# Optimization experiments

Measured on AMD Instinct MI355X. Metric: run time of the kernel, lower is better.

## Reference

```python
import jax, jax.numpy as jnp
import numpy as np

NUM_EXPERTS = 8
TOP_K = 2
LORA_ALPHA = 2.0
LORA_RANK = 16
D_MODEL = 2048
D_HIDDEN = 5632


def setup_inputs() -> dict:
    key = jax.random.key(0)
    ks = jax.random.split(key, 11)
    B, S, D, H, E, R = 2, 1024, D_MODEL, D_HIDDEN, NUM_EXPERTS, LORA_RANK
    sd = 1.0 / np.sqrt(D)
    sh = 1.0 / np.sqrt(H)
    x = jax.random.normal(ks[0], (B, S, D), jnp.float32)
    gate_w = jax.random.normal(ks[1], (E, D), jnp.float32) * sd   # router Linear(D->E), no bias
    w_up = jax.random.normal(ks[2], (H, D), jnp.float32) * sd     # up_proj.weight
    w_gate = jax.random.normal(ks[3], (H, D), jnp.float32) * sd   # gate_proj.weight
    w_down = jax.random.normal(ks[4], (D, H), jnp.float32) * sh   # down_proj.weight
    up_A = jax.random.normal(ks[5], (E, R, D), jnp.float32) * sd
    up_B = jax.random.normal(ks[6], (E, H, R), jnp.float32) * 0.02
    gate_A = jax.random.normal(ks[7], (E, R, D), jnp.float32) * sd
    gate_B = jax.random.normal(ks[8], (E, H, R), jnp.float32) * 0.02
    down_A = jax.random.normal(ks[9], (E, R, H), jnp.float32) * sh
    down_B = jax.random.normal(ks[10], (E, D, R), jnp.float32) * 0.02
    return {"x": x, "gate_w": gate_w, "w_up": w_up, "w_gate": w_gate,
            "w_down": w_down, "up_A": up_A, "up_B": up_B,
            "gate_A": gate_A, "gate_B": gate_B, "down_A": down_A, "down_B": down_B}


def reference(x, gate_w, w_up, w_gate, w_down, up_A, up_B, gate_A, gate_B, down_A, down_B):
    B, S, D = x.shape
    H = w_up.shape[0]
    # router: logits [B,S,E], top-k over experts (last dim)
    gate_logits = jnp.einsum('bsd,ed->bse', x, gate_w)
    topw, sel = jax.lax.top_k(gate_logits, TOP_K)            # [B,S,k]
    # NOTE: source applies softmax over dim=1 (the SEQUENCE axis) -- reproduced faithfully
    topw = jax.nn.softmax(topw.astype(jnp.float32), axis=1).astype(x.dtype)
    xt = x.reshape(-1, D)                                    # [T, D]
    wf = topw.reshape(-1, TOP_K)                             # [T, k]
    sf = sel.reshape(-1, TOP_K)                              # [T, k]
    # shared base projections computed once for all tokens
    base_up = xt @ w_up.T                                    # [T, H]
    base_gate = xt @ w_gate.T                                # [T, H]
    mixed_h = jnp.zeros((xt.shape[0], H), x.dtype)
    lora_down = jnp.zeros_like(xt)
    # loop over fixed small expert count; low-rank LoRA deltas applied without
    # materializing full merged weights (same math by linearity of matmul)
    for e in range(NUM_EXPERTS):
        c = jnp.sum(jnp.where(sf == e, wf, 0.0), axis=1)     # [T] routing weight (0 if not routed)
        lo_up = LORA_ALPHA * ((xt @ up_A[e].T) @ up_B[e].T)
        lo_gate = LORA_ALPHA * ((xt @ gate_A[e].T) @ gate_B[e].T)
        h_e = jax.nn.silu(base_up + lo_up) * (base_gate + lo_gate)  # [T, H]
        ch = c[:, None] * h_e
        mixed_h = mixed_h + ch
        lora_down = lora_down + LORA_ALPHA * ((ch @ down_A[e].T) @ down_B[e].T)
    out = mixed_h @ w_down.T + lora_down                     # base down GEMM done once on mixed hidden
    return out.reshape(B, S, D)
```

## Files before the change

kernel.cpp:

```cpp
#include <hip/hip_runtime.h>
#include <hip/hip_fp16.h>
#include <cmath>

#define TOKENS 2048
#define DMODEL 2048
#define DHID   5632
#define NEXP   8
#define RANK   16
#define LALPHA 2.0f

typedef __attribute__((ext_vector_type(4))) float f32x4;
typedef __attribute__((ext_vector_type(8))) short s16x8;
typedef __attribute__((ext_vector_type(4))) short s16x4;
typedef __attribute__((ext_vector_type(8))) _Float16 f16x8;

__device__ __forceinline__ short f2bf(float f){
  unsigned u = __float_as_uint(f);
  u += 0x7fffu + ((u >> 16) & 1u);
  return (short)(u >> 16);
}
__device__ __forceinline__ short f2h(float f){
  return (short)__half_as_ushort(__float2half(f));
}

struct Src2 { const short* s0; const short* s1; };

__device__ __forceinline__ Src2 mk_src(const short* g, long ld, int tid){
  Src2 st;
  const int L0 = tid,      r0 = L0>>2, c0 = ((L0&3) - (r0>>1)) & 3;
  const int L1 = 256+tid,  r1 = L1>>2, c1 = ((L1&3) - (r1>>1)) & 3;
  st.s0 = g + (long)r0*ld + c0*8;
  st.s1 = g + (long)r1*ld + c1*8;
  return st;
}
__device__ __forceinline__ void stage2(const Src2& st, int k0, short* t, int tid){
  __builtin_amdgcn_global_load_lds((const __attribute__((address_space(1))) void*)(st.s0 + k0),
                                   (__attribute__((address_space(3))) void*)(t + tid*8), 16, 0, 0);
  __builtin_amdgcn_global_load_lds((const __attribute__((address_space(1))) void*)(st.s1 + k0),
                                   (__attribute__((address_space(3))) void*)(t + (256+tid)*8), 16, 0, 0);
}
__device__ __forceinline__ s16x8 fragb(const short* t, int row, int quad){
  const int p = (quad + (row>>1)) & 3;
  return *(const s16x8*)(t + (row*4 + p)*8);
}
__device__ __forceinline__ f16x8 fragh(const short* t, int row, int quad){
  const int p = (quad + (row>>1)) & 3;
  return *(const f16x8*)(t + (row*4 + p)*8);
}

struct Stage64 { const short* g; short* t; int off[4]; int dof; };

__device__ __forceinline__ Stage64 mk_stage64(const short* g, long ld, short* t, int tid){
  Stage64 st; st.g = g; st.t = t;
  #pragma unroll
  for(int p=0;p<4;p++){
    const int L = p*256 + tid;
    const int r = L>>3, cp = L&7;
    const int c = (cp - (r&7)) & 7;
    st.off[p] = r*(int)ld + c*8;
  }
  st.dof = tid*8;
  return st;
}
__device__ __forceinline__ void do_stage64(const Stage64& st, int k0){
  #pragma unroll
  for(int p=0;p<4;p++)
    __builtin_amdgcn_global_load_lds(
      (const __attribute__((address_space(1))) void*)(st.g + st.off[p] + k0),
      (__attribute__((address_space(3))) void*)(st.t + st.dof + p*2048), 16, 0, 0);
}
__device__ __forceinline__ s16x8 fragb64(const short* t, int row, int ksub, int quad){
  const int c = ksub*4 + quad;
  const int p = (c + (row&7)) & 7;
  return *(const s16x8*)(t + (row*8 + p)*8);
}
__device__ __forceinline__ f16x8 fragh64(const short* t, int row, int ksub, int quad){
  const int c = ksub*4 + quad;
  const int p = (c + (row&7)) & 7;
  return *(const f16x8*)(t + (row*8 + p)*8);
}

__global__ void k_cast(const float* __restrict__ x, const float* __restrict__ w_up,
                       const float* __restrict__ w_gate, const float* __restrict__ w_down,
                       const float* __restrict__ upA, const float* __restrict__ gateA,
                       const float* __restrict__ downA, const float* __restrict__ upB,
                       const float* __restrict__ gateB, const float* __restrict__ downB,
                       short* __restrict__ xb, short* __restrict__ wub, short* __restrict__ wgb,
                       short* __restrict__ wdb, short* __restrict__ daA, short* __restrict__ acat,
                       short* __restrict__ upBcat, short* __restrict__ gateBcat, short* __restrict__ wdbcat){
  const long e0 = 4194304, e1 = 15728640, e2 = 27262976, e3 = 38797312;
  const long e4 = 39518208, e5 = 40042496, e6 = 40763392, e7 = 41484288, e8 = 41746432;
  const long i = ((long)blockIdx.x*256 + threadIdx.x) * 4;
  if(i >= e8) return;
  const float* src; short* dst; long l; int fp16 = 0;
  if(i < e0){ src = x; dst = xb; l = i; }
  else if(i < e1){ src = w_up; dst = wub; l = i - e0; }
  else if(i < e2){ src = w_gate; dst = wgb; l = i - e1; }
  else if(i < e3){ src = w_down; dst = wdb; l = i - e2; }
  else if(i < e4){ src = downA; dst = daA; l = i - e3; }
  else if(i < e5){
    l = i - e4;
    const long c = l>>11;
    const long e = c>>5, pj = (c>>4)&1, r = c&15;
    src = (pj ? gateA : upA) + ((e*RANK + r)<<11) + (l&2047) - l;
    dst = acat;
  }
  else if(i < e6){
    l = i - e5;
    const long h = l>>7, c = l&127, e = c>>4, r = c&15;
    src = upB + ((e*DHID + h)*RANK + r) - l;
    dst = upBcat; fp16 = 1;
  }
  else if(i < e7){
    l = i - e6;
    const long h = l>>7, c = l&127, e = c>>4, r = c&15;
    src = gateB + ((e*DHID + h)*RANK + r) - l;
    dst = gateBcat; fp16 = 1;
  }
  else {
    l = i - e7;
    const long d = l>>7, c = l&127, e = c>>4, r = c&15;
    src = downB + ((e*DMODEL + d)*RANK + r) - l;
    dst = wdbcat; fp16 = 1;
  }
  const float4 v = *(const float4*)(src + l);
  s16x4 o;
  if(fp16){ o[0]=f2h(v.x); o[1]=f2h(v.y); o[2]=f2h(v.z); o[3]=f2h(v.w); }
  else    { o[0]=f2bf(v.x); o[1]=f2bf(v.y); o[2]=f2bf(v.z); o[3]=f2bf(v.w); }
  *(s16x4*)(dst + l) = o;
}

__global__ void k_router(const float* __restrict__ x, const float* __restrict__ gw,
                         int* __restrict__ sel, float* __restrict__ topv){
  const int t = blockIdx.x*4 + (threadIdx.x>>6);
  const int lane = threadIdx.x & 63;
  const float* xr = x + (long)t * DMODEL;
  float acc[NEXP];
  #pragma unroll
  for(int e=0;e<NEXP;e++) acc[e]=0.f;
  #pragma unroll
  for(int it=0; it<8; it++){
    const int d = it*256 + lane*4;
    const float4 xv = *(const float4*)(xr + d);
    #pragma unroll
    for(int e=0;e<NEXP;e++){
      const float4 wv = *(const float4*)(gw + e*DMODEL + d);
      acc[e] += xv.x*wv.x + xv.y*wv.y + xv.z*wv.z + xv.w*wv.w;
    }
  }
  #pragma unroll
  for(int e=0;e<NEXP;e++){
    #pragma unroll
    for(int off=32; off; off>>=1) acc[e] += __shfl_down(acc[e], off, 64);
  }
  if(lane==0){
    int i0=0;
    #pragma unroll
    for(int e=1;e<NEXP;e++) if(acc[e]>acc[i0]) i0=e;
    int i1=-1;
    #pragma unroll
    for(int e=0;e<NEXP;e++){ if(e==i0) continue; if(i1<0 || acc[e]>acc[i1]) i1=e; }
    sel[t*2+0]=i0; sel[t*2+1]=i1;
    topv[t*2+0]=acc[i0]; topv[t*2+1]=acc[i1];
  }
}

__global__ void k_softmax(const float* __restrict__ topv, float* __restrict__ cw){
  const int b = blockIdx.x >> 1, k = blockIdx.x & 1;
  const int base = b*1024;
  __shared__ float red[256];
  float v[4];
  float mx = -1e30f;
  #pragma unroll
  for(int i=0;i<4;i++){
    int s = threadIdx.x + i*256;
    v[i] = topv[(base+s)*2 + k];
    mx = fmaxf(mx, v[i]);
  }
  red[threadIdx.x]=mx; __syncthreads();
  for(int o=128;o;o>>=1){ if(threadIdx.x<o) red[threadIdx.x]=fmaxf(red[threadIdx.x],red[threadIdx.x+o]); __syncthreads(); }
  mx = red[0]; __syncthreads();
  float sum=0.f;
  #pragma unroll
  for(int i=0;i<4;i++){ v[i]=__expf(v[i]-mx); sum+=v[i]; }
  red[threadIdx.x]=sum; __syncthreads();
  for(int o=128;o;o>>=1){ if(threadIdx.x<o) red[threadIdx.x]+=red[threadIdx.x+o]; __syncthreads(); }
  const float inv = 1.f/red[0];
  #pragma unroll
  for(int i=0;i<4;i++){
    int s = threadIdx.x + i*256;
    cw[(base+s)*2+k] = v[i]*inv;
  }
}

__global__ __launch_bounds__(256,2) void k_rank(
    const short* __restrict__ xb, const short* __restrict__ acat, float* __restrict__ Rall){
  __shared__ __align__(16) short At[8192];
  __shared__ __align__(16) short Bt[8192];
  const int c0 = blockIdx.x*128, t0 = blockIdx.y*128;
  const int kbeg = blockIdx.z*256;
  const int tid = threadIdx.x, lane = tid&63, wave = tid>>6;
  const int wm=(wave>>1)*64, wn=(wave&1)*64, fr=lane&15, quad=lane>>4;
  f32x4 acc[4][4];
  #pragma unroll
  for(int i=0;i<4;i++)
    #pragma unroll
    for(int j=0;j<4;j++) acc[i][j]=(f32x4){0.f,0.f,0.f,0.f};
  const Stage64 sA = mk_stage64(xb + (long)t0*DMODEL, DMODEL, At, tid);
  const Stage64 sB = mk_stage64(acat + (long)c0*DMODEL, DMODEL, Bt, tid);
  for(int k0=kbeg; k0<kbeg+256; k0+=64){
    do_stage64(sA, k0); do_stage64(sB, k0);
    __syncthreads();
    #pragma unroll
    for(int s=0;s<2;s++){
      s16x8 af[4];
      #pragma unroll
      for(int i=0;i<4;i++) af[i] = fragb64(At, wm + i*16 + fr, s, quad);
      #pragma unroll
      for(int j=0;j<4;j++){
        const s16x8 bf = fragb64(Bt, wn + j*16 + fr, s, quad);
        #pragma unroll
        for(int i=0;i<4;i++)
          acc[i][j] = __builtin_amdgcn_mfma_f32_16x16x32_bf16(af[i], bf, acc[i][j], 0,0,0);
      }
    }
    __syncthreads();
  }
  #pragma unroll
  for(int i=0;i<4;i++)
    #pragma unroll
    for(int j=0;j<4;j++){
      const int rbase = wm + i*16 + quad*4, col = wn + j*16 + fr;
      #pragma unroll
      for(int reg=0;reg<4;reg++)
        atomicAdd(&Rall[(long)(t0+rbase+reg)*256 + c0 + col], acc[i][j][reg]);
    }
}

__global__ void k_rsel(const float* __restrict__ Rall, const int* __restrict__ sel,
                       short* __restrict__ RselU, short* __restrict__ RselG){
  const int idx = blockIdx.x*256 + threadIdx.x;
  const int c = idx & 127, t = (idx>>7) & (TOKENS-1), k = idx>>18;
  const int e = c>>4, r = c&15;
  const int s = sel[t*2+k];
  const int m = (e==s);
  RselU[idx] = f2h(m ? LALPHA*Rall[(long)t*256 + e*32 + r]      : 0.f);
  RselG[idx] = f2h(m ? LALPHA*Rall[(long)t*256 + e*32 + 16 + r] : 0.f);
}

__global__ __launch_bounds__(256,2) void k_lora(
    const short* __restrict__ RselU, const short* __restrict__ RselG,
    const short* __restrict__ upBcat, const short* __restrict__ gateBcat,
    short* __restrict__ LF){
  __shared__ __align__(16) short At[8192];
  __shared__ __align__(16) short Gt[8192];
  __shared__ __align__(16) short Bt[8192];
  const int h0 = blockIdx.x*128, t0 = blockIdx.y*128;
  const short* Rsel = blockIdx.z ? RselG : RselU;
  const short* Bcat = blockIdx.z ? gateBcat : upBcat;
  const int tid = threadIdx.x, lane = tid&63, wave = tid>>6;
  const int wm=(wave>>1)*64, wn=(wave&1)*64, fr=lane&15, quad=lane>>4;
  f32x4 l0[4][4], l1[4][4];
  #pragma unroll
  for(int i=0;i<4;i++)
    #pragma unroll
    for(int j=0;j<4;j++){ l0[i][j]=(f32x4){0.f,0.f,0.f,0.f}; l1[i][j]=l0[i][j]; }
  const Stage64 sB  = mk_stage64(Bcat + (long)h0*128, 128, Bt, tid);
  const Stage64 sR0 = mk_stage64(Rsel + (long)t0*128, 128, At, tid);
  const Stage64 sR1 = mk_stage64(Rsel + ((long)TOKENS + t0)*128, 128, Gt, tid);
  for(int k0=0; k0<128; k0+=64){
    do_stage64(sB, k0); do_stage64(sR0, k0); do_stage64(sR1, k0);
    __syncthreads();
    #pragma unroll
    for(int s=0;s<2;s++){
      f16x8 a0[4], a1[4];
      #pragma unroll
      for(int i=0;i<4;i++){ a0[i] = fragh64(At, wm + i*16 + fr, s, quad);
                            a1[i] = fragh64(Gt, wm + i*16 + fr, s, quad); }
      #pragma unroll
      for(int j=0;j<4;j++){
        const f16x8 bf = fragh64(Bt, wn + j*16 + fr, s, quad);
        #pragma unroll
        for(int i=0;i<4;i++){
          l0[i][j] = __builtin_amdgcn_mfma_f32_16x16x32_f16(a0[i], bf, l0[i][j], 0,0,0);
          l1[i][j] = __builtin_amdgcn_mfma_f32_16x16x32_f16(a1[i], bf, l1[i][j], 0,0,0);
        }
      }
    }
    __syncthreads();
  }
  short* o = LF + (long)(blockIdx.y*44 + blockIdx.x)*65536 + ((long)blockIdx.z*16*256 + tid)*8;
  #pragma unroll
  for(int i=0;i<4;i++){
    s16x8 p0a, p0b, p1a, p1b;
    #pragma unroll
    for(int r=0;r<4;r++){
      p0a[r]   = f2h(l0[i][0][r]); p0a[4+r] = f2h(l0[i][1][r]);
      p0b[r]   = f2h(l0[i][2][r]); p0b[4+r] = f2h(l0[i][3][r]);
      p1a[r]   = f2h(l1[i][0][r]); p1a[4+r] = f2h(l1[i][1][r]);
      p1b[r]   = f2h(l1[i][2][r]); p1b[4+r] = f2h(l1[i][3][r]);
    }
    *(s16x8*)(o + (i*2+0)*2048)     = p0a;
    *(s16x8*)(o + (i*2+1)*2048)     = p0b;
    *(s16x8*)(o + (8 + i*2+0)*2048) = p1a;
    *(s16x8*)(o + (8 + i*2+1)*2048) = p1b;
  }
}

__global__ __launch_bounds__(256,2) void k_main(
    const short* __restrict__ xb, const short* __restrict__ wub, const short* __restrict__ wgb,
    const short* __restrict__ LF,
    const float* __restrict__ cw, unsigned short* __restrict__ ch, unsigned short* __restrict__ chsum){
  __shared__ __align__(16) short At[2][4096];
  __shared__ __align__(16) short Ut[2][4096];
  __shared__ __align__(16) short Gt[2][4096];
  __shared__ float cwv[128][2];
  const int h0 = blockIdx.x*128, t0 = blockIdx.y*128;
  const int tid = threadIdx.x, lane = tid&63, wave = tid>>6;
  const int wm=(wave>>1)*64, wn=(wave&1)*64, fr=lane&15, quad=lane>>4;
  { const int tl = tid>>1, k = tid&1; cwv[tl][k] = cw[(t0+tl)*2 + k]; }
  f32x4 au[4][4], ag[4][4];
  #pragma unroll
  for(int i=0;i<4;i++)
    #pragma unroll
    for(int j=0;j<4;j++){ au[i][j]=(f32x4){0.f,0.f,0.f,0.f}; ag[i][j]=au[i][j]; }
  const Src2 sA = mk_src(xb + (long)t0*DMODEL, DMODEL, tid);
  const Src2 sU = mk_src(wub + (long)h0*DMODEL, DMODEL, tid);
  const Src2 sG = mk_src(wgb + (long)h0*DMODEL, DMODEL, tid);
  stage2(sA, 0, At[0], tid); stage2(sU, 0, Ut[0], tid); stage2(sG, 0, Gt[0], tid);
  __syncthreads();
  int cur = 0;
  for(int k0=0; k0<DMODEL; k0+=32){
    const int nxt = cur^1;
    if(k0+32 < DMODEL){
      stage2(sA, k0+32, At[nxt], tid);
      stage2(sU, k0+32, Ut[nxt], tid);
      stage2(sG, k0+32, Gt[nxt], tid);
    }
    __builtin_amdgcn_sched_barrier(0);
    s16x8 af[4];
    #pragma unroll
    for(int i=0;i<4;i++) af[i] = fragb(At[cur], wm + i*16 + fr, quad);
    #pragma unroll
    for(int j=0;j<4;j++){
      const s16x8 bu = fragb(Ut[cur], wn + j*16 + fr, quad);
      const s16x8 bg = fragb(Gt[cur], wn + j*16 + fr, quad);
      #pragma unroll
      for(int i=0;i<4;i++){
        au[i][j] = __builtin_amdgcn_mfma_f32_16x16x32_bf16(af[i], bu, au[i][j], 0,0,0);
        ag[i][j] = __builtin_amdgcn_mfma_f32_16x16x32_bf16(af[i], bg, ag[i][j], 0,0,0);
      }
    }
    __syncthreads();
    cur = nxt;
  }
  const short* Lf = LF + (long)(blockIdx.y*44 + blockIdx.x)*65536 + (long)tid*8;
  #pragma unroll
  for(int i=0;i<4;i++){
    f16x8 Uv0[2], Uv1[2], Gv0[2], Gv1[2];
    Uv0[0] = *(const f16x8*)(Lf + (i*2+0)*2048);       Uv0[1] = *(const f16x8*)(Lf + (i*2+1)*2048);
    Uv1[0] = *(const f16x8*)(Lf + (8+i*2+0)*2048);     Uv1[1] = *(const f16x8*)(Lf + (8+i*2+1)*2048);
    Gv0[0] = *(const f16x8*)(Lf + (16+i*2+0)*2048);    Gv0[1] = *(const f16x8*)(Lf + (16+i*2+1)*2048);
    Gv1[0] = *(const f16x8*)(Lf + (24+i*2+0)*2048);    Gv1[1] = *(const f16x8*)(Lf + (24+i*2+1)*2048);
    #pragma unroll
    for(int reg=0;reg<4;reg++){
      const int tl = wm + i*16 + quad*4 + reg;
      const float c0 = cwv[tl][0], c1 = cwv[tl][1];
      const long row0 = (long)(t0+tl)*DHID + h0;
      const long row1 = ((long)TOKENS + t0+tl)*DHID + h0;
      unsigned short* r0 = ch + row0;
      unsigned short* r1 = ch + row1;
      unsigned short* rs = chsum + row0;
      #pragma unroll
      for(int j=0;j<4;j++){
        const int hl = wn + j*16 + fr;
        const int q = (j&1)*4 + reg, hv = j>>1;
        const float u0 = au[i][j][reg] + (float)Uv0[hv][q];
        const float g0 = ag[i][j][reg] + (float)Gv0[hv][q];
        const float h0v = (u0 / (1.f + __expf(-u0))) * g0;
        const float u1 = au[i][j][reg] + (float)Uv1[hv][q];
        const float g1 = ag[i][j][reg] + (float)Gv1[hv][q];
        const float h1v = (u1 / (1.f + __expf(-u1))) * g1;
        const float v0 = c0*h0v, v1 = c1*h1v;
        r0[hl] = (unsigned short)f2bf(v0);
        r1[hl] = (unsigned short)f2bf(v1);
        rs[hl] = (unsigned short)f2bf(v0+v1);
      }
    }
  }
}

__global__ __launch_bounds__(256,4) void k_rd(
    const unsigned short* __restrict__ ch, const short* __restrict__ daA,
    float* __restrict__ RD){
  __shared__ __align__(16) short At[4096];
  __shared__ __align__(16) short Bt[4096];
  const int slot = blockIdx.x>>4, ks = blockIdx.x&15;
  const int t0 = blockIdx.y*128;
  const int tid = threadIdx.x, lane = tid&63, wave = tid>>6;
  const int wm=(wave>>1)*64, wn=(wave&1)*64, fr=lane&15, quad=lane>>4;
  f32x4 acc[4][4];
  #pragma unroll
  for(int i=0;i<4;i++)
    #pragma unroll
    for(int j=0;j<4;j++) acc[i][j]=(f32x4){0.f,0.f,0.f,0.f};
  const Src2 sA = mk_src((const short*)ch + ((long)slot*TOKENS + t0)*DHID, DHID, tid);
  const Src2 sB = mk_src(daA, DHID, tid);
  const int kbeg = ks*352;
  for(int kk=0; kk<352; kk+=32){
    stage2(sA, kbeg+kk, At, tid); stage2(sB, kbeg+kk, Bt, tid);
    __syncthreads();
    s16x8 af[4];
    #pragma unroll
    for(int i=0;i<4;i++) af[i] = fragb(At, wm + i*16 + fr, quad);
    #pragma unroll
    for(int j=0;j<4;j++){
      const s16x8 bf = fragb(Bt, wn + j*16 + fr, quad);
      #pragma unroll
      for(int i=0;i<4;i++)
        acc[i][j] = __builtin_amdgcn_mfma_f32_16x16x32_bf16(af[i], bf, acc[i][j], 0,0,0);
    }
    __syncthreads();
  }
  #pragma unroll
  for(int i=0;i<4;i++)
    #pragma unroll
    for(int j=0;j<4;j++){
      const int rbase = wm + i*16 + quad*4, col = wn + j*16 + fr;
      #pragma unroll
      for(int reg=0;reg<4;reg++)
        atomicAdd(&RD[((long)(t0+rbase+reg)*2 + slot)*128 + col], acc[i][j][reg]);
    }
}

__global__ void k_scatter(const float* __restrict__ RD, const int* __restrict__ sel,
                          __half* __restrict__ RDhat){
  const int idx = blockIdx.x*256 + threadIdx.x;
  const int t = idx>>7, c = idx&127, e = c>>4;
  const int s0 = sel[t*2], s1 = sel[t*2+1];
  float v = 0.f;
  if(e == s0) v = LALPHA * RD[((long)t*2+0)*128 + c];
  else if(e == s1) v = LALPHA * RD[((long)t*2+1)*128 + c];
  RDhat[idx] = __float2half(v);
}

__global__ __launch_bounds__(256,2) void k_down(
    const unsigned short* __restrict__ chsum, const short* __restrict__ wdb,
    const short* __restrict__ RDhat, const short* __restrict__ wdbcat,
    float* __restrict__ out){
  __shared__ __align__(16) short At[2][4096];
  __shared__ __align__(16) short Bt[2][4096];
  const int d0 = blockIdx.x*128, t0 = blockIdx.y*128, ks = blockIdx.z;
  const int tid = threadIdx.x, lane = tid&63, wave = tid>>6;
  const int wm=(wave>>1)*64, wn=(wave&1)*64, fr=lane&15, quad=lane>>4;
  f32x4 acc[4][4];
  #pragma unroll
  for(int i=0;i<4;i++)
    #pragma unroll
    for(int j=0;j<4;j++) acc[i][j]=(f32x4){0.f,0.f,0.f,0.f};
  const Src2 sA = mk_src((const short*)chsum + (long)t0*DHID, DHID, tid);
  const Src2 sB = mk_src(wdb + (long)d0*DHID, DHID, tid);
  const int kbeg = ks*2816;
  stage2(sA, kbeg, At[0], tid); stage2(sB, kbeg, Bt[0], tid);
  __syncthreads();
  int cur = 0;
  for(int kk=0; kk<2816; kk+=32){
    const int nxt = cur^1;
    if(kk+32 < 2816){
      stage2(sA, kbeg+kk+32, At[nxt], tid);
      stage2(sB, kbeg+kk+32, Bt[nxt], tid);
    }
    __builtin_amdgcn_sched_barrier(0);
    s16x8 af[4];
    #pragma unroll
    for(int i=0;i<4;i++) af[i] = fragb(At[cur], wm + i*16 + fr, quad);
    #pragma unroll
    for(int j=0;j<4;j++){
      const s16x8 bf = fragb(Bt[cur], wn + j*16 + fr, quad);
      #pragma unroll
      for(int i=0;i<4;i++)
        acc[i][j] = __builtin_amdgcn_mfma_f32_16x16x32_bf16(af[i], bf, acc[i][j], 0,0,0);
    }
    __syncthreads();
    cur = nxt;
  }
  if(ks == 0){
    const Src2 sAh = mk_src(RDhat + (long)t0*128, 128, tid);
    const Src2 sBh = mk_src(wdbcat + (long)d0*128, 128, tid);
    stage2(sAh, 0, At[cur], tid); stage2(sBh, 0, Bt[cur], tid);
    __syncthreads();
    for(int k0=0; k0<128; k0+=32){
      const int nxt = cur^1;
      if(k0+32 < 128){
        stage2(sAh, k0+32, At[nxt], tid);
        stage2(sBh, k0+32, Bt[nxt], tid);
      }
      __builtin_amdgcn_sched_barrier(0);
      f16x8 af[4];
      #pragma unroll
      for(int i=0;i<4;i++) af[i] = fragh(At[cur], wm + i*16 + fr, quad);
      #pragma unroll
      for(int j=0;j<4;j++){
        const f16x8 bf = fragh(Bt[cur], wn + j*16 + fr, quad);
        #pragma unroll
        for(int i=0;i<4;i++)
          acc[i][j] = __builtin_amdgcn_mfma_f32_16x16x32_f16(af[i], bf, acc[i][j], 0,0,0);
      }
      __syncthreads();
      cur = nxt;
    }
  }
  #pragma unroll
  for(int i=0;i<4;i++)
    #pragma unroll
    for(int j=0;j<4;j++){
      const int rbase = wm + i*16 + quad*4, col = wn + j*16 + fr;
      #pragma unroll
      for(int reg=0;reg<4;reg++)
        atomicAdd(&out[(long)(t0+rbase+reg)*DMODEL + d0 + col], acc[i][j][reg]);
    }
}

extern "C" void kernel_launch(void* const* d_in, const int* in_sizes, int n_in,
                              void* d_out, int out_size, void* d_ws, size_t ws_size,
                              hipStream_t stream){
  (void)in_sizes; (void)n_in; (void)out_size; (void)ws_size;
  const float* x      = (const float*)d_in[0];
  const float* gate_w = (const float*)d_in[1];
  const float* w_up   = (const float*)d_in[2];
  const float* w_gate = (const float*)d_in[3];
  const float* w_down = (const float*)d_in[4];
  const float* up_A   = (const float*)d_in[5];
  const float* up_B   = (const float*)d_in[6];
  const float* gate_A = (const float*)d_in[7];
  const float* gate_B = (const float*)d_in[8];
  const float* down_A = (const float*)d_in[9];
  const float* down_B = (const float*)d_in[10];
  float* out = (float*)d_out;

  char* ws = (char*)d_ws;
  size_t off = 0;
  auto alloc = [&](size_t bytes){ void* p = ws + off; off += (bytes + 255) & ~(size_t)255; return p; };
  short* xb       = (short*)alloc((size_t)TOKENS*DMODEL*2);
  short* wub      = (short*)alloc((size_t)DHID*DMODEL*2);
  short* wgb      = (short*)alloc((size_t)DHID*DMODEL*2);
  short* wdb      = (short*)alloc((size_t)DMODEL*DHID*2);
  short* daA      = (short*)alloc((size_t)128*DHID*2);
  short* acat     = (short*)alloc((size_t)256*DMODEL*2);
  short* upBcat   = (short*)alloc((size_t)DHID*128*2);
  short* gateBcat = (short*)alloc((size_t)DHID*128*2);
  short* wdbcat   = (short*)alloc((size_t)DMODEL*128*2);
  unsigned short* ch    = (unsigned short*)alloc((size_t)2*TOKENS*DHID*2);
  unsigned short* chsum = (unsigned short*)alloc((size_t)TOKENS*DHID*2);
  short* LF     = (short*)alloc((size_t)704*65536*2);
  float* Rall   = (float*)alloc((size_t)TOKENS*256*4);
  short* RselU  = (short*)alloc((size_t)2*TOKENS*128*2);
  short* RselG  = (short*)alloc((size_t)2*TOKENS*128*2);
  float* RD     = (float*)alloc((size_t)TOKENS*2*128*4);
  __half* RDhat = (__half*)alloc((size_t)TOKENS*128*2);
  int*   sel    = (int*)alloc((size_t)TOKENS*2*4);
  float* topv   = (float*)alloc((size_t)TOKENS*2*4);
  float* cw     = (float*)alloc((size_t)TOKENS*2*4);

  (void)hipMemsetAsync(RD, 0, (size_t)TOKENS*2*128*4, stream);
  (void)hipMemsetAsync(Rall, 0, (size_t)TOKENS*256*4, stream);
  (void)hipMemsetAsync(out, 0, (size_t)TOKENS*DMODEL*4, stream);
  k_cast<<<40768, 256, 0, stream>>>(x, w_up, w_gate, w_down, up_A, gate_A, down_A,
                                    up_B, gate_B, down_B,
                                    xb, wub, wgb, wdb, daA, acat, upBcat, gateBcat, wdbcat);
  k_router<<<512, 256, 0, stream>>>(x, gate_w, sel, topv);
  k_softmax<<<4, 256, 0, stream>>>(topv, cw);
  k_rank<<<dim3(2,16,8), 256, 0, stream>>>(xb, acat, Rall);
  k_rsel<<<2048, 256, 0, stream>>>(Rall, sel, RselU, RselG);
  k_lora<<<dim3(44,16,2), 256, 0, stream>>>(RselU, RselG, upBcat, gateBcat, LF);
  k_main<<<dim3(44,16), 256, 0, stream>>>(xb, wub, wgb, LF, cw, ch, chsum);
  k_rd<<<dim3(32,16), 256, 0, stream>>>(ch, daA, RD);
  k_scatter<<<1024, 256, 0, stream>>>(RD, sel, RDhat);
  k_down<<<dim3(16,16,2), 256, 0, stream>>>(chsum, wdb, (const short*)RDhat, wdbcat, out);
}
```

Before: 538.9 us.

## Triple-buffer LDS staging with explicit vmcnt waits in main, rd and down GEMMs

Replaces the double-buffered global-to-LDS pipelines in the fused up/gate, LoRA reduce and down-projection kernels with a three-stage ring buffer. Explicit s_waitcnt vmcnt counts plus raw barriers let two tile loads stay in flight while the current tile is consumed, so memory latency is hidden deeper. The routing-weight shared-memory table in the main kernel is dropped in favour of direct global loads in the epilogue, and k_rd's launch bounds drop to 2 blocks per CU. The larger LDS footprint may reduce occupancy, and the hand-coded wait counts depend on how many loads stage2 issues.

```diff
diff --git a/kernel.cpp b/kernel.cpp
--- a/kernel.cpp
+++ b/kernel.cpp
@@ -311,14 +311,12 @@
     const short* __restrict__ xb, const short* __restrict__ wub, const short* __restrict__ wgb,
     const short* __restrict__ LF,
     const float* __restrict__ cw, unsigned short* __restrict__ ch, unsigned short* __restrict__ chsum){
-  __shared__ __align__(16) short At[2][4096];
-  __shared__ __align__(16) short Ut[2][4096];
-  __shared__ __align__(16) short Gt[2][4096];
-  __shared__ float cwv[128][2];
+  __shared__ __align__(16) short At[3][4096];
+  __shared__ __align__(16) short Ut[3][4096];
+  __shared__ __align__(16) short Gt[3][4096];
   const int h0 = blockIdx.x*128, t0 = blockIdx.y*128;
   const int tid = threadIdx.x, lane = tid&63, wave = tid>>6;
   const int wm=(wave>>1)*64, wn=(wave&1)*64, fr=lane&15, quad=lane>>4;
-  { const int tl = tid>>1, k = tid&1; cwv[tl][k] = cw[(t0+tl)*2 + k]; }
   f32x4 au[4][4], ag[4][4];
   #pragma unroll
   for(int i=0;i<4;i++)
@@ -327,33 +325,53 @@
   const Src2 sA = mk_src(xb + (long)t0*DMODEL, DMODEL, tid);
   const Src2 sU = mk_src(wub + (long)h0*DMODEL, DMODEL, tid);
   const Src2 sG = mk_src(wgb + (long)h0*DMODEL, DMODEL, tid);
-  stage2(sA, 0, At[0], tid); stage2(sU, 0, Ut[0], tid); stage2(sG, 0, Gt[0], tid);
-  __syncthreads();
-  int cur = 0;
-  for(int k0=0; k0<DMODEL; k0+=32){
-    const int nxt = cur^1;
-    if(k0+32 < DMODEL){
-      stage2(sA, k0+32, At[nxt], tid);
-      stage2(sU, k0+32, Ut[nxt], tid);
-      stage2(sG, k0+32, Gt[nxt], tid);
-    }
-    __builtin_amdgcn_sched_barrier(0);
+
+  auto kstep = [&](const short* A, const short* U, const short* G){
     s16x8 af[4];
     #pragma unroll
-    for(int i=0;i<4;i++) af[i] = fragb(At[cur], wm + i*16 + fr, quad);
+    for(int i=0;i<4;i++) af[i] = fragb(A, wm + i*16 + fr, quad);
     #pragma unroll
     for(int j=0;j<4;j++){
-      const s16x8 bu = fragb(Ut[cur], wn + j*16 + fr, quad);
-      const s16x8 bg = fragb(Gt[cur], wn + j*16 + fr, quad);
+      const s16x8 bu = fragb(U, wn + j*16 + fr, quad);
+      const s16x8 bg = fragb(G, wn + j*16 + fr, quad);
       #pragma unroll
       for(int i=0;i<4;i++){
         au[i][j] = __builtin_amdgcn_mfma_f32_16x16x32_bf16(af[i], bu, au[i][j], 0,0,0);
         ag[i][j] = __builtin_amdgcn_mfma_f32_16x16x32_bf16(af[i], bg, ag[i][j], 0,0,0);
       }
     }
-    __syncthreads();
-    cur = nxt;
-  }
+  };
+
+  short *A0=At[0], *A1=At[1], *A2=At[2];
+  short *U0=Ut[0], *U1=Ut[1], *U2=Ut[2];
+  short *G0=Gt[0], *G1=Gt[1], *G2=Gt[2];
+  stage2(sA, 0,  A0, tid); stage2(sU, 0,  U0, tid); stage2(sG, 0,  G0, tid);
+  stage2(sA, 32, A1, tid); stage2(sU, 32, U1, tid); stage2(sG, 32, G1, tid);
+  for(int s=0; s<62; s++){
+    const int k2 = (s+2)*32;
+    stage2(sA, k2, A2, tid); stage2(sU, k2, U2, tid); stage2(sG, k2, G2, tid);
+    asm volatile("s_waitcnt vmcnt(12)" ::: "memory");
+    __builtin_amdgcn_s_barrier();
+    __builtin_amdgcn_sched_barrier(0);
+    kstep(A0, U0, G0);
+    __builtin_amdgcn_sched_barrier(0);
+    __builtin_amdgcn_s_barrier();
+    short* t;
+    t=A0; A0=A1; A1=A2; A2=t;
+    t=U0; U0=U1; U1=U2; U2=t;
+    t=G0; G0=G1; G1=G2; G2=t;
+  }
+  asm volatile("s_waitcnt vmcnt(6)" ::: "memory");
+  __builtin_amdgcn_s_barrier();
+  __builtin_amdgcn_sched_barrier(0);
+  kstep(A0, U0, G0);
+  __builtin_amdgcn_sched_barrier(0);
+  __builtin_amdgcn_s_barrier();
+  asm volatile("s_waitcnt vmcnt(0)" ::: "memory");
+  __builtin_amdgcn_s_barrier();
+  __builtin_amdgcn_sched_barrier(0);
+  kstep(A1, U1, G1);
+
   const short* Lf = LF + (long)(blockIdx.y*44 + blockIdx.x)*65536 + (long)tid*8;
   #pragma unroll
   for(int i=0;i<4;i++){
@@ -365,7 +383,8 @@
     #pragma unroll
     for(int reg=0;reg<4;reg++){
       const int tl = wm + i*16 + quad*4 + reg;
-      const float c0 = cwv[tl][0], c1 = cwv[tl][1];
+      const float2 cc = *(const float2*)(cw + (long)(t0+tl)*2);
+      const float c0 = cc.x, c1 = cc.y;
       const long row0 = (long)(t0+tl)*DHID + h0;
       const long row1 = ((long)TOKENS + t0+tl)*DHID + h0;
       unsigned short* r0 = ch + row0;
@@ -390,11 +409,11 @@
   }
 }
 
-__global__ __launch_bounds__(256,4) void k_rd(
+__global__ __launch_bounds__(256,2) void k_rd(
     const unsigned short* __restrict__ ch, const short* __restrict__ daA,
     float* __restrict__ RD){
-  __shared__ __align__(16) short At[4096];
-  __shared__ __align__(16) short Bt[4096];
+  __shared__ __align__(16) short At[3][4096];
+  __shared__ __align__(16) short Bt[3][4096];
   const int slot = blockIdx.x>>4, ks = blockIdx.x&15;
   const int t0 = blockIdx.y*128;
   const int tid = threadIdx.x, lane = tid&63, wave = tid>>6;
@@ -407,21 +426,48 @@
   const Src2 sA = mk_src((const short*)ch + ((long)slot*TOKENS + t0)*DHID, DHID, tid);
   const Src2 sB = mk_src(daA, DHID, tid);
   const int kbeg = ks*352;
-  for(int kk=0; kk<352; kk+=32){
-    stage2(sA, kbeg+kk, At, tid); stage2(sB, kbeg+kk, Bt, tid);
-    __syncthreads();
+
+  auto kstep = [&](const short* A, const short* B){
     s16x8 af[4];
     #pragma unroll
-    for(int i=0;i<4;i++) af[i] = fragb(At, wm + i*16 + fr, quad);
+    for(int i=0;i<4;i++) af[i] = fragb(A, wm + i*16 + fr, quad);
     #pragma unroll
     for(int j=0;j<4;j++){
-      const s16x8 bf = fragb(Bt, wn + j*16 + fr, quad);
+      const s16x8 bf = fragb(B, wn + j*16 + fr, quad);
       #pragma unroll
       for(int i=0;i<4;i++)
         acc[i][j] = __builtin_amdgcn_mfma_f32_16x16x32_bf16(af[i], bf, acc[i][j], 0,0,0);
     }
-    __syncthreads();
-  }
+  };
+
+  short *A0=At[0], *A1=At[1], *A2=At[2];
+  short *B0=Bt[0], *B1=Bt[1], *B2=Bt[2];
+  stage2(sA, kbeg,    A0, tid); stage2(sB, kbeg,    B0, tid);
+  stage2(sA, kbeg+32, A1, tid); stage2(sB, kbeg+32, B1, tid);
+  for(int s=0; s<9; s++){
+    const int k2 = kbeg + (s+2)*32;
+    stage2(sA, k2, A2, tid); stage2(sB, k2, B2, tid);
+    asm volatile("s_waitcnt vmcnt(8)" ::: "memory");
+    __builtin_amdgcn_s_barrier();
+    __builtin_amdgcn_sched_barrier(0);
+    kstep(A0, B0);
+    __builtin_amdgcn_sched_barrier(0);
+    __builtin_amdgcn_s_barrier();
+    short* t;
+    t=A0; A0=A1; A1=A2; A2=t;
+    t=B0; B0=B1; B1=B2; B2=t;
+  }
+  asm volatile("s_waitcnt vmcnt(4)" ::: "memory");
+  __builtin_amdgcn_s_barrier();
+  __builtin_amdgcn_sched_barrier(0);
+  kstep(A0, B0);
+  __builtin_amdgcn_sched_barrier(0);
+  __builtin_amdgcn_s_barrier();
+  asm volatile("s_waitcnt vmcnt(0)" ::: "memory");
+  __builtin_amdgcn_s_barrier();
+  __builtin_amdgcn_sched_barrier(0);
+  kstep(A1, B1);
+
   #pragma unroll
   for(int i=0;i<4;i++)
     #pragma unroll
@@ -448,8 +494,8 @@
     const unsigned short* __restrict__ chsum, const short* __restrict__ wdb,
     const short* __restrict__ RDhat, const short* __restrict__ wdbcat,
     float* __restrict__ out){
-  __shared__ __align__(16) short At[2][4096];
-  __shared__ __align__(16) short Bt[2][4096];
+  __shared__ __align__(16) short At[3][4096];
+  __shared__ __align__(16) short Bt[3][4096];
   const int d0 = blockIdx.x*128, t0 = blockIdx.y*128, ks = blockIdx.z;
   const int tid = threadIdx.x, lane = tid&63, wave = tid>>6;
   const int wm=(wave>>1)*64, wn=(wave&1)*64, fr=lane&15, quad=lane>>4;
@@ -461,34 +507,55 @@
   const Src2 sA = mk_src((const short*)chsum + (long)t0*DHID, DHID, tid);
   const Src2 sB = mk_src(wdb + (long)d0*DHID, DHID, tid);
   const int kbeg = ks*2816;
-  stage2(sA, kbeg, At[0], tid); stage2(sB, kbeg, Bt[0], tid);
-  __syncthreads();
-  int cur = 0;
-  for(int kk=0; kk<2816; kk+=32){
-    const int nxt = cur^1;
-    if(kk+32 < 2816){
-      stage2(sA, kbeg+kk+32, At[nxt], tid);
-      stage2(sB, kbeg+kk+32, Bt[nxt], tid);
-    }
-    __builtin_amdgcn_sched_barrier(0);
+
+  auto kstep = [&](const short* A, const short* B){
     s16x8 af[4];
     #pragma unroll
-    for(int i=0;i<4;i++) af[i] = fragb(At[cur], wm + i*16 + fr, quad);
+    for(int i=0;i<4;i++) af[i] = fragb(A, wm + i*16 + fr, quad);
     #pragma unroll
     for(int j=0;j<4;j++){
-      const s16x8 bf = fragb(Bt[cur], wn + j*16 + fr, quad);
+      const s16x8 bf = fragb(B, wn + j*16 + fr, quad);
       #pragma unroll
       for(int i=0;i<4;i++)
         acc[i][j] = __builtin_amdgcn_mfma_f32_16x16x32_bf16(af[i], bf, acc[i][j], 0,0,0);
     }
-    __syncthreads();
-    cur = nxt;
-  }
+  };
+
+  short *A0=At[0], *A1=At[1], *A2=At[2];
+  short *B0=Bt[0], *B1=Bt[1], *B2=Bt[2];
+  stage2(sA, kbeg,    A0, tid); stage2(sB, kbeg,    B0, tid);
+  stage2(sA, kbeg+32, A1, tid); stage2(sB, kbeg+32, B1, tid);
+  for(int s=0; s<86; s++){
+    const int k2 = kbeg + (s+2)*32;
+    stage2(sA, k2, A2, tid); stage2(sB, k2, B2, tid);
+    asm volatile("s_waitcnt vmcnt(8)" ::: "memory");
+    __builtin_amdgcn_s_barrier();
+    __builtin_amdgcn_sched_barrier(0);
+    kstep(A0, B0);
+    __builtin_amdgcn_sched_barrier(0);
+    __builtin_amdgcn_s_barrier();
+    short* t;
+    t=A0; A0=A1; A1=A2; A2=t;
+    t=B0; B0=B1; B1=B2; B2=t;
+  }
+  asm volatile("s_waitcnt vmcnt(4)" ::: "memory");
+  __builtin_amdgcn_s_barrier();
+  __builtin_amdgcn_sched_barrier(0);
+  kstep(A0, B0);
+  __builtin_amdgcn_sched_barrier(0);
+  __builtin_amdgcn_s_barrier();
+  asm volatile("s_waitcnt vmcnt(0)" ::: "memory");
+  __builtin_amdgcn_s_barrier();
+  __builtin_amdgcn_sched_barrier(0);
+  kstep(A1, B1);
+  __builtin_amdgcn_s_barrier();
+
   if(ks == 0){
     const Src2 sAh = mk_src(RDhat + (long)t0*128, 128, tid);
     const Src2 sBh = mk_src(wdbcat + (long)d0*128, 128, tid);
-    stage2(sAh, 0, At[cur], tid); stage2(sBh, 0, Bt[cur], tid);
+    stage2(sAh, 0, At[0], tid); stage2(sBh, 0, Bt[0], tid);
     __syncthreads();
+    int cur = 0;
     for(int k0=0; k0<128; k0+=32){
       const int nxt = cur^1;
       if(k0+32 < 128){
```

After: 537.9 us. About the same (-0.2%).
